# Kernel tuning notes

Hardware: AMD Instinct MI355X
Metric: run time of the kernel (lower is better)

The kernel has to match this reference:

```python
import jax, jax.numpy as jnp
import numpy as np

WH, WW = 8, 8          # window height/width
NUM_HEADS = 12


def _rel_tables():
    # continuous relative coords table, shape (1, 2*WH-1, 2*WW-1, 2)
    rh = np.arange(-(WH - 1), WH, dtype=np.float32)
    rw = np.arange(-(WW - 1), WW, dtype=np.float32)
    t = np.expand_dims(np.transpose(np.stack(np.meshgrid(rh, rw)), (1, 2, 0)), axis=0)
    t[:, :, :, 0] /= WH - 1
    t[:, :, :, 1] /= WW - 1
    t *= 8
    table = np.sign(t) * np.log2(np.abs(t) + 1.0) / np.log2(8)
    # relative position index, shape (WH*WW, WH*WW), values in [0, (2WH-1)*(2WW-1))
    ch = np.arange(WH)
    cw = np.arange(WW)
    x, y = np.meshgrid(ch, cw)
    coords = np.stack([y, x]).reshape(2, -1)
    rc = coords[:, :, None] - coords[:, None, :]
    rc = np.transpose(rc, (1, 2, 0))
    rc[:, :, 0] += WH - 1
    rc[:, :, 1] += WW - 1
    rc[:, :, 0] *= 2 * WW - 1
    idx = rc.sum(-1)
    return jnp.asarray(table, dtype=jnp.float32), jnp.asarray(idx, dtype=jnp.int32)


_REL_TABLE, _REL_IDX = _rel_tables()


def setup_inputs() -> dict:
    key = jax.random.key(0)
    ks = jax.random.split(key, 10)
    B_, N, C = 1152, 64, 384
    s = 1.0 / np.sqrt(C)
    return {
        "x": jax.random.normal(ks[0], (B_, N, C), jnp.float32),
        "mask": jnp.zeros((B_, N, N), jnp.float32),  # nW == B_ (B=1)
        "wq": jax.random.normal(ks[1], (C, C), jnp.float32) * s,
        "bq": jnp.zeros((C,), jnp.float32),
        "wk": jax.random.normal(ks[2], (C, C), jnp.float32) * s,
        "wv": jax.random.normal(ks[3], (C, C), jnp.float32) * s,
        "bv": jnp.zeros((C,), jnp.float32),
        "cpb_w1": jax.random.normal(ks[4], (2, 512), jnp.float32) * 0.5,
        "cpb_b1": jnp.zeros((512,), jnp.float32),
        "cpb_w2": jax.random.normal(ks[5], (512, NUM_HEADS), jnp.float32) * (1.0 / np.sqrt(512)),
        "cpb_b2": jnp.zeros((NUM_HEADS,), jnp.float32),
        "tau": jax.random.normal(ks[6], (1, NUM_HEADS, 1, 1), jnp.float32) * 0.02,
        "wproj": jax.random.normal(ks[7], (C, C), jnp.float32) * s,
        "bproj": jnp.zeros((C,), jnp.float32),
    }


def reference(x, mask, wq, bq, wk, wv, bv, cpb_w1, cpb_b1, cpb_w2, cpb_b2, tau, wproj, bproj):
    B_, N, C = x.shape
    H = NUM_HEADS
    Dh = C // H

    def heads(t):  # (B_, N, C) -> (B_, H, N, Dh)
        return jnp.transpose(t.reshape(B_, N, H, Dh), (0, 2, 1, 3))

    q = heads(x @ wq + bq)
    k = heads(x @ wk)
    v = heads(x @ wv + bv)

    # cosine attention: normalize by |q||k|, clamp denominator
    qn = jnp.linalg.norm(q, axis=-1)  # (B_, H, N)
    kn = jnp.linalg.norm(k, axis=-1)
    denom = jnp.maximum(qn[..., :, None] * kn[..., None, :], 1e-6)
    logit_scale = jnp.maximum(tau + jnp.log(10.0), 0.01)  # (1, H, 1, 1)
    attn = jnp.einsum('bhnd,bhmd->bhnm', q, k) / denom * logit_scale

    # continuous position bias via small MLP + gather by relative index
    tb = jax.nn.relu(_REL_TABLE @ cpb_w1 + cpb_b1) @ cpb_w2 + cpb_b2  # (1,15,15,H)
    tb = tb.reshape(-1, H)  # (225, H)
    bias = tb[_REL_IDX.reshape(-1)].reshape(N, N, H)
    bias = 16.0 * jax.nn.sigmoid(jnp.transpose(bias, (2, 0, 1)))  # (H, N, N)
    attn = attn + bias[None]

    nW = mask.shape[0]
    attn = (attn.reshape(B_ // nW, nW, H, N, N) + mask[None, :, None]).reshape(B_, H, N, N)
    attn = jax.nn.softmax(attn, axis=-1)

    out = jnp.transpose(jnp.einsum('bhnm,bhmd->bhnd', attn, v), (0, 2, 1, 3)).reshape(B_, N, C)
    return out @ wproj + bproj
```

## Files before the change

### kernel.cpp

```cpp
#include <hip/hip_runtime.h>
#include <math.h>

#define NB   1152
#define NTOK 64
#define NC   384
#define NH   12
#define NDH  32

typedef short short8 __attribute__((ext_vector_type(8)));
typedef float f32x4  __attribute__((ext_vector_type(4)));

__device__ __forceinline__ unsigned short f2bf(float f) {
    unsigned int u = __builtin_bit_cast(unsigned int, f);
    unsigned int r = u + 0x7fffu + ((u >> 16) & 1u);
    return (unsigned short)(r >> 16);
}
__device__ __forceinline__ unsigned int pack2(float lo, float hi) {
    return (unsigned int)f2bf(lo) | ((unsigned int)f2bf(hi) << 16);
}
__device__ __forceinline__ f32x4 mfma_bf16(short8 a, short8 b, f32x4 c) {
    return __builtin_amdgcn_mfma_f32_16x16x32_bf16(a, b, c, 0, 0, 0);
}

__device__ __forceinline__ short8 tile_afrag(const unsigned short* t, int row, int kq) {
    return *(const short8*)((const char*)t + row * 768 + ((kq ^ (row & 7)) << 4));
}

__device__ __forceinline__ short8 repack_frag(f32x4 a0, f32x4 a1, int Q, int t) {
    unsigned p00 = pack2(a0[0], a0[1]);
    unsigned p01 = pack2(a0[2], a0[3]);
    unsigned p10 = pack2(a1[0], a1[1]);
    unsigned p11 = pack2(a1[2], a1[3]);
    const int s0 = ((Q & 1) << 5) + t;
    const int s1 = s0 + 16;
    int u0a = __shfl((int)p00, s0, 64), u0b = __shfl((int)p10, s0, 64);
    int u1a = __shfl((int)p01, s0, 64), u1b = __shfl((int)p11, s0, 64);
    int u2a = __shfl((int)p00, s1, 64), u2b = __shfl((int)p10, s1, 64);
    int u3a = __shfl((int)p01, s1, 64), u3b = __shfl((int)p11, s1, 64);
    const bool hi = (Q & 2) != 0;
    uint4 u;
    u.x = (unsigned)(hi ? u0b : u0a);
    u.y = (unsigned)(hi ? u1b : u1a);
    u.z = (unsigned)(hi ? u2b : u2a);
    u.w = (unsigned)(hi ? u3b : u3a);
    return __builtin_bit_cast(short8, u);
}

__global__ __launch_bounds__(256) void prep_kernel(
    const float* __restrict__ wq, const float* __restrict__ wk,
    const float* __restrict__ wv, const float* __restrict__ wproj,
    unsigned int* __restrict__ wT, unsigned int* __restrict__ wprojT)
{
    const int o2 = blockIdx.x * 256 + threadIdx.x;
    if (o2 < 221184) {
        const int col = o2 / 192, k2 = o2 % 192, k = k2 * 2;
        const float* src = (col < 384) ? wq : ((col < 768) ? wk : wv);
        const int c = (col < 384) ? col : ((col < 768) ? col - 384 : col - 768);
        const float a = src[(size_t)k * NC + c];
        const float b = src[(size_t)(k + 1) * NC + c];
        wT[col * 192 + k2] = pack2(a, b);
    } else {
        const int o = o2 - 221184;
        const int col = o / 192, k2 = o % 192, k = k2 * 2;
        const float a = wproj[(size_t)k * NC + col];
        const float b = wproj[(size_t)(k + 1) * NC + col];
        wprojT[col * 192 + k2] = pack2(a, b);
    }
}

__global__ __launch_bounds__(64) void cpb_mlp_kernel(
    const float* __restrict__ w1, const float* __restrict__ b1,
    const float* __restrict__ w2, const float* __restrict__ b2,
    float* __restrict__ tbs)
{
    const int p = blockIdx.x;
    const int lane = threadIdx.x;
    const int ip = p / 15, jp = p % 15;
    float u0 = (float)(jp - 7) * (8.0f / 7.0f);
    float u1 = (float)(ip - 7) * (8.0f / 7.0f);
    float s0 = (u0 > 0.f) ? 1.f : ((u0 < 0.f) ? -1.f : 0.f);
    float s1 = (u1 > 0.f) ? 1.f : ((u1 < 0.f) ? -1.f : 0.f);
    float in0 = s0 * log2f(fabsf(u0) + 1.0f) * (1.0f / 3.0f);
    float in1 = s1 * log2f(fabsf(u1) + 1.0f) * (1.0f / 3.0f);

    float a[12];
    #pragma unroll
    for (int m = 0; m < 12; ++m) a[m] = 0.f;
    #pragma unroll
    for (int e = 0; e < 8; ++e) {
        const int j = lane * 8 + e;
        float hh = fmaxf(in0 * w1[j] + in1 * w1[512 + j] + b1[j], 0.0f);
        #pragma unroll
        for (int m = 0; m < 12; ++m) a[m] += hh * w2[j * 12 + m];
    }
    #pragma unroll
    for (int m = 0; m < 12; ++m) {
        #pragma unroll
        for (int off = 1; off < 64; off <<= 1) a[m] += __shfl_xor(a[m], off, 64);
    }
    if (lane < 12) tbs[p * 12 + lane] = a[lane] + b2[lane];
}

__global__ __launch_bounds__(1024) void bias_gather_kernel(
    const float* __restrict__ tbs, float* __restrict__ bias)
{
    const int i = blockIdx.x * 1024 + threadIdx.x;
    if (i >= NH * NTOK * NTOK) return;
    const int h = i >> 12, rem = i & 4095;
    const int ti = rem >> 6, tj = rem & 63;
    const int dr = (ti >> 3) - (tj >> 3);
    const int dc = (ti & 7) - (tj & 7);
    const int p = (dr + 7) * 15 + (dc + 7);
    bias[i] = 16.0f / (1.0f + __expf(-tbs[p * 12 + h]));
}

__global__ __launch_bounds__(256, 2) void attn_kernel(
    const float* __restrict__ x,    const float* __restrict__ mask,
    const float* __restrict__ bq,   const float* __restrict__ bv,
    const float* __restrict__ tau,  const unsigned short* __restrict__ wT,
    const float* __restrict__ bias, float* __restrict__ out)
{
    __shared__ unsigned short xs[64 * 384];
    __shared__ unsigned short vTs[4][32 * 72];
    __shared__ unsigned short Pss[4][16 * 72];

    const int tid = threadIdx.x;
    const int b   = blockIdx.x;
    const int w   = tid >> 6;
    const int lane = tid & 63;
    const int Q   = lane >> 4;
    const int t   = lane & 15;

    unsigned int* xsu = (unsigned int*)xs;

    float maskv[4][4];
    #pragma unroll
    for (int nt = 0; nt < 4; ++nt)
        #pragma unroll
        for (int r = 0; r < 4; ++r)
            maskv[nt][r] = mask[(size_t)b * 4096 + (Q * 4 + r) * 64 + nt * 16 + t];
    (void)maskv;

    {
        const int row = tid >> 2;
        const int q4  = tid & 3;
        const float* xr = &x[((size_t)b * NTOK + row) * NC + q4 * 96];
        #pragma unroll
        for (int e = 0; e < 24; ++e) {
            const float4 xv = *(const float4*)&xr[e * 4];
            const int p = q4 * 48 + e * 2;
            const int g = p >> 2;
            const int u = row * 192 + (((g ^ (row & 7)) << 2) | (p & 3));
            uint2 w2;
            w2.x = pack2(xv.x, xv.y);
            w2.y = pack2(xv.z, xv.w);
            *(uint2*)&xsu[u] = w2;
        }
    }
    __syncthreads();

    unsigned short* vT = vTs[w];
    unsigned short* Ps = Pss[w];

    for (int c = 0; c < 3; ++c) {
        const int h = w * 3 + c;

        f32x4 acckv[4][4];
        #pragma unroll
        for (int j = 0; j < 4; ++j)
            #pragma unroll
            for (int tt = 0; tt < 4; ++tt) acckv[j][tt] = (f32x4){0.f, 0.f, 0.f, 0.f};

        {
            const unsigned short* ap[4];
            #pragma unroll
            for (int j = 0; j < 4; ++j) {
                const int cbase = (1 + (j >> 1)) * 384 + h * 32 + (j & 1) * 16;
                ap[j] = wT + (size_t)(cbase + t) * NC + Q * 8;
            }
            for (int ks = 0; ks < 12; ++ks) {
                short8 bfr[4];
                #pragma unroll
                for (int tt = 0; tt < 4; ++tt)
                    bfr[tt] = tile_afrag(xs, tt * 16 + t, ks * 4 + Q);
                #pragma unroll
                for (int j = 0; j < 4; ++j) {
                    const short8 af = *(const short8*)&ap[j][ks * 32];
                    #pragma unroll
                    for (int tt = 0; tt < 4; ++tt)
                        acckv[j][tt] = mfma_bf16(af, bfr[tt], acckv[j][tt]);
                }
            }
        }

        #pragma unroll
        for (int a = 0; a < 2; ++a) {
            #pragma unroll
            for (int r = 0; r < 4; ++r) {
                const float bvv = bv[h * 32 + a * 16 + Q * 4 + r];
                #pragma unroll
                for (int tt = 0; tt < 4; ++tt)
                    vT[(a * 16 + Q * 4 + r) * 72 + tt * 16 + t]
                        = f2bf(acckv[2 + a][tt][r] + bvv);
            }
        }

        float kn[4];
        #pragma unroll
        for (int tt = 0; tt < 4; ++tt) {
            float sk = 0.f;
            #pragma unroll
            for (int a = 0; a < 2; ++a)
                #pragma unroll
                for (int r = 0; r < 4; ++r)
                    sk += acckv[a][tt][r] * acckv[a][tt][r];
            sk += __shfl_xor(sk, 16, 64);
            sk += __shfl_xor(sk, 32, 64);
            kn[tt] = sqrtf(sk);
        }

        short8 bk[4];
        #pragma unroll
        for (int nt = 0; nt < 4; ++nt)
            bk[nt] = repack_frag(acckv[0][nt], acckv[1][nt], Q, t);

        short8 vf[2][2];
        #pragma unroll
        for (int n = 0; n < 2; ++n)
            #pragma unroll
            for (int st = 0; st < 2; ++st)
                vf[n][st] = *(const short8*)&vT[(n * 16 + t) * 72 + st * 32 + Q * 8];

        f32x4 accq[2][4];
        #pragma unroll
        for (int a = 0; a < 2; ++a)
            #pragma unroll
            for (int tt = 0; tt < 4; ++tt) accq[a][tt] = (f32x4){0.f, 0.f, 0.f, 0.f};

        {
            const unsigned short* ap[2];
            #pragma unroll
            for (int a = 0; a < 2; ++a)
                ap[a] = wT + (size_t)(h * 32 + a * 16 + t) * NC + Q * 8;
            for (int ks = 0; ks < 12; ++ks) {
                short8 bfr[4];
                #pragma unroll
                for (int tt = 0; tt < 4; ++tt)
                    bfr[tt] = tile_afrag(xs, tt * 16 + t, ks * 4 + Q);
                #pragma unroll
                for (int a = 0; a < 2; ++a) {
                    const short8 af = *(const short8*)&ap[a][ks * 32];
                    #pragma unroll
                    for (int tt = 0; tt < 4; ++tt)
                        accq[a][tt] = mfma_bf16(af, bfr[tt], accq[a][tt]);
                }
            }
        }

        float qn[4];
        short8 aqf[4];
        #pragma unroll
        for (int a = 0; a < 2; ++a) {
            #pragma unroll
            for (int r = 0; r < 4; ++r) {
                const float bqv = bq[h * 32 + a * 16 + Q * 4 + r];
                #pragma unroll
                for (int tt = 0; tt < 4; ++tt) accq[a][tt][r] += bqv;
            }
        }
        #pragma unroll
        for (int tt = 0; tt < 4; ++tt) {
            float sq = 0.f;
            #pragma unroll
            for (int a = 0; a < 2; ++a)
                #pragma unroll
                for (int r = 0; r < 4; ++r)
                    sq += accq[a][tt][r] * accq[a][tt][r];
            sq += __shfl_xor(sq, 16, 64);
            sq += __shfl_xor(sq, 32, 64);
            qn[tt] = sqrtf(sq);
            aqf[tt] = repack_frag(accq[0][tt], accq[1][tt], Q, t);
        }

        const float ls = fmaxf(tau[h] + 2.302585093f, 0.01f);

        #pragma unroll
        for (int mt = 0; mt < 4; ++mt) {
            float bmv[4][4];
            #pragma unroll
            for (int nt = 0; nt < 4; ++nt)
                #pragma unroll
                for (int r = 0; r < 4; ++r) {
                    const int row = mt * 16 + Q * 4 + r;
                    const int col = nt * 16 + t;
                    bmv[nt][r] = bias[h * 4096 + row * 64 + col]
                               + mask[(size_t)b * 4096 + row * 64 + col];
                }

            float qr[4];
            #pragma unroll
            for (int r = 0; r < 4; ++r) qr[r] = __shfl(qn[mt], Q * 4 + r, 64);

            float svf[4][4];
            #pragma unroll
            for (int nt = 0; nt < 4; ++nt) {
                const f32x4 sv = mfma_bf16(aqf[mt], bk[nt], (f32x4){0.f, 0.f, 0.f, 0.f});
                #pragma unroll
                for (int r = 0; r < 4; ++r) {
                    const float den = fmaxf(qr[r] * kn[nt], 1e-6f);
                    svf[nt][r] = sv[r] / den * ls + bmv[nt][r];
                }
            }

            float mx[4], sm[4];
            #pragma unroll
            for (int r = 0; r < 4; ++r) {
                float m = fmaxf(fmaxf(svf[0][r], svf[1][r]), fmaxf(svf[2][r], svf[3][r]));
                #pragma unroll
                for (int off = 1; off < 16; off <<= 1) m = fmaxf(m, __shfl_xor(m, off, 64));
                mx[r] = m; sm[r] = 0.f;
            }
            #pragma unroll
            for (int nt = 0; nt < 4; ++nt)
                #pragma unroll
                for (int r = 0; r < 4; ++r) {
                    const float e = __expf(svf[nt][r] - mx[r]);
                    svf[nt][r] = e; sm[r] += e;
                }
            #pragma unroll
            for (int r = 0; r < 4; ++r) {
                #pragma unroll
                for (int off = 1; off < 16; off <<= 1) sm[r] += __shfl_xor(sm[r], off, 64);
            }

            #pragma unroll
            for (int nt = 0; nt < 4; ++nt)
                #pragma unroll
                for (int r = 0; r < 4; ++r)
                    Ps[(Q * 4 + r) * 72 + nt * 16 + t] = f2bf(svf[nt][r]);

            f32x4 oa[2];
            oa[0] = (f32x4){0.f, 0.f, 0.f, 0.f};
            oa[1] = (f32x4){0.f, 0.f, 0.f, 0.f};
            #pragma unroll
            for (int st = 0; st < 2; ++st) {
                const short8 apf = *(const short8*)&Ps[t * 72 + st * 32 + Q * 8];
                #pragma unroll
                for (int n = 0; n < 2; ++n)
                    oa[n] = mfma_bf16(apf, vf[n][st], oa[n]);
            }

            float rsi[4];
            #pragma unroll
            for (int r = 0; r < 4; ++r) rsi[r] = 1.0f / sm[r];
            #pragma unroll
            for (int n = 0; n < 2; ++n)
                #pragma unroll
                for (int r = 0; r < 4; ++r)
                    out[((size_t)b * NTOK + mt * 16 + Q * 4 + r) * NC + h * 32 + n * 16 + t]
                        = oa[n][r] * rsi[r];
        }
    }
}

__global__ __launch_bounds__(256) void proj_kernel(
    const unsigned short* __restrict__ wprojT, const float* __restrict__ bproj,
    float* __restrict__ out)
{
    __shared__ unsigned short as_[64 * 384];
    unsigned int* asu = (unsigned int*)as_;

    const int tid  = threadIdx.x;
    const size_t r0 = (size_t)blockIdx.x * 64;
    const int w    = tid >> 6;
    const int lane = tid & 63;
    const int quad = lane >> 4;
    const int lq   = lane & 15;

    {
        const int row = tid >> 2;
        const int q4  = tid & 3;
        const float* xr = &out[(r0 + row) * NC + q4 * 96];
        #pragma unroll
        for (int e = 0; e < 24; ++e) {
            const float4 xv = *(const float4*)&xr[e * 4];
            const int p = q4 * 48 + e * 2;
            const int g = p >> 2;
            const int u = row * 192 + (((g ^ (row & 7)) << 2) | (p & 3));
            uint2 w2;
            w2.x = pack2(xv.x, xv.y);
            w2.y = pack2(xv.z, xv.w);
            *(uint2*)&asu[u] = w2;
        }
    }
    __syncthreads();

    f32x4 acc[4][6];
    #pragma unroll
    for (int mt = 0; mt < 4; ++mt)
        #pragma unroll
        for (int n = 0; n < 6; ++n) acc[mt][n] = (f32x4){0.f, 0.f, 0.f, 0.f};

    const unsigned short* bp[6];
    #pragma unroll
    for (int n = 0; n < 6; ++n)
        bp[n] = wprojT + (size_t)(w * 96 + n * 16 + lq) * NC + quad * 8;

    for (int ksI = 0; ksI < 12; ++ksI) {
        short8 am[4];
        #pragma unroll
        for (int mt = 0; mt < 4; ++mt)
            am[mt] = tile_afrag(as_, mt * 16 + lq, ksI * 4 + quad);
        #pragma unroll
        for (int n = 0; n < 6; ++n) {
            const short8 bb = *(const short8*)&bp[n][ksI * 32];
            #pragma unroll
            for (int mt = 0; mt < 4; ++mt) acc[mt][n] = mfma_bf16(am[mt], bb, acc[mt][n]);
        }
    }

    float bpv[6];
    #pragma unroll
    for (int n = 0; n < 6; ++n) bpv[n] = bproj[w * 96 + n * 16 + lq];
    #pragma unroll
    for (int mt = 0; mt < 4; ++mt)
        #pragma unroll
        for (int n = 0; n < 6; ++n)
            #pragma unroll
            for (int r = 0; r < 4; ++r)
                out[(r0 + mt * 16 + quad * 4 + r) * NC + w * 96 + n * 16 + lq]
                    = acc[mt][n][r] + bpv[n];
}

extern "C" void kernel_launch(void* const* d_in, const int* in_sizes, int n_in,
                              void* d_out, int out_size, void* d_ws, size_t ws_size,
                              hipStream_t stream) {
    (void)in_sizes; (void)n_in; (void)out_size; (void)ws_size;
    const float* x     = (const float*)d_in[0];
    const float* mask  = (const float*)d_in[1];
    const float* wq    = (const float*)d_in[2];
    const float* bq    = (const float*)d_in[3];
    const float* wk    = (const float*)d_in[4];
    const float* wv    = (const float*)d_in[5];
    const float* bv    = (const float*)d_in[6];
    const float* w1    = (const float*)d_in[7];
    const float* b1    = (const float*)d_in[8];
    const float* w2    = (const float*)d_in[9];
    const float* b2    = (const float*)d_in[10];
    const float* tau   = (const float*)d_in[11];
    const float* wproj = (const float*)d_in[12];
    const float* bproj = (const float*)d_in[13];
    float* out = (float*)d_out;

    unsigned short* wT     = (unsigned short*)d_ws;
    unsigned short* wprojT = (unsigned short*)((char*)d_ws + 884736);
    float*          bias   = (float*)((char*)d_ws + 884736 + 294912);
    float*          tbs    = (float*)((char*)d_ws + 884736 + 294912 + 196608);

    prep_kernel<<<1152, 256, 0, stream>>>(wq, wk, wv, wproj,
                                          (unsigned int*)wT, (unsigned int*)wprojT);
    cpb_mlp_kernel<<<225, 64, 0, stream>>>(w1, b1, w2, b2, tbs);
    bias_gather_kernel<<<48, 1024, 0, stream>>>(tbs, bias);
    attn_kernel<<<NB, 256, 0, stream>>>(x, mask, bq, bv, tau, wT, bias, out);
    proj_kernel<<<NB, 256, 0, stream>>>(wprojT, bproj, out);
}
```

Measured before the change: 631.4 us.

## Compute attention in transposed MFMA layout to keep P and V in registers

The attention kernel now computes S^T, V^T and O^T by swapping MFMA operands. Each lane then owns a whole query row, so the softmax max and sum reductions shrink to two cross-lane shuffles, and P and V fragments are repacked in registers instead of going through per-wave LDS buffers. Bias and mask loads and output stores become float4-vectorised, and the occupancy hint rises from 2 to 3 blocks per CU. The trade-off is more repack work and register pressure, which could cause spills under the tighter launch bound.

Result: slower. 812.2 us (+28.6%).

```diff
diff --git a/kernel.cpp b/kernel.cpp
--- a/kernel.cpp
+++ b/kernel.cpp
@@ -114,32 +114,22 @@
     bias[i] = 16.0f / (1.0f + __expf(-tbs[p * 12 + h]));
 }
 
-__global__ __launch_bounds__(256, 2) void attn_kernel(
+__global__ __launch_bounds__(256, 3) void attn_kernel(
     const float* __restrict__ x,    const float* __restrict__ mask,
     const float* __restrict__ bq,   const float* __restrict__ bv,
     const float* __restrict__ tau,  const unsigned short* __restrict__ wT,
     const float* __restrict__ bias, float* __restrict__ out)
 {
     __shared__ unsigned short xs[64 * 384];
-    __shared__ unsigned short vTs[4][32 * 72];
-    __shared__ unsigned short Pss[4][16 * 72];
-
-    const int tid = threadIdx.x;
-    const int b   = blockIdx.x;
-    const int w   = tid >> 6;
+
+    const int tid  = threadIdx.x;
+    const int b    = blockIdx.x;
+    const int w    = tid >> 6;
     const int lane = tid & 63;
-    const int Q   = lane >> 4;
-    const int t   = lane & 15;
+    const int Q    = lane >> 4;
+    const int t    = lane & 15;
 
     unsigned int* xsu = (unsigned int*)xs;
-
-    float maskv[4][4];
-    #pragma unroll
-    for (int nt = 0; nt < 4; ++nt)
-        #pragma unroll
-        for (int r = 0; r < 4; ++r)
-            maskv[nt][r] = mask[(size_t)b * 4096 + (Q * 4 + r) * 64 + nt * 16 + t];
-    (void)maskv;
 
     {
         const int row = tid >> 2;
@@ -159,24 +149,22 @@
     }
     __syncthreads();
 
-    unsigned short* vT = vTs[w];
-    unsigned short* Ps = Pss[w];
-
     for (int c = 0; c < 3; ++c) {
         const int h = w * 3 + c;
 
-        f32x4 acckv[4][4];
+        f32x4 akv[4][4];
         #pragma unroll
         for (int j = 0; j < 4; ++j)
             #pragma unroll
-            for (int tt = 0; tt < 4; ++tt) acckv[j][tt] = (f32x4){0.f, 0.f, 0.f, 0.f};
+            for (int tt = 0; tt < 4; ++tt) akv[j][tt] = (f32x4){0.f, 0.f, 0.f, 0.f};
 
         {
-            const unsigned short* ap[4];
-            #pragma unroll
-            for (int j = 0; j < 4; ++j) {
-                const int cbase = (1 + (j >> 1)) * 384 + h * 32 + (j & 1) * 16;
-                ap[j] = wT + (size_t)(cbase + t) * NC + Q * 8;
+            const unsigned short* apk[2];
+            const unsigned short* apv[2];
+            #pragma unroll
+            for (int a = 0; a < 2; ++a) {
+                apk[a] = wT + (size_t)(384 + h * 32 + a * 16 + t) * NC + Q * 8;
+                apv[a] = wT + (size_t)(768 + h * 32 + a * 16 + t) * NC + Q * 8;
             }
             for (int ks = 0; ks < 12; ++ks) {
                 short8 bfr[4];
@@ -184,25 +172,29 @@
                 for (int tt = 0; tt < 4; ++tt)
                     bfr[tt] = tile_afrag(xs, tt * 16 + t, ks * 4 + Q);
                 #pragma unroll
-                for (int j = 0; j < 4; ++j) {
-                    const short8 af = *(const short8*)&ap[j][ks * 32];
+                for (int a = 0; a < 2; ++a) {
+                    const short8 afk = *(const short8*)&apk[a][ks * 32];
                     #pragma unroll
                     for (int tt = 0; tt < 4; ++tt)
-                        acckv[j][tt] = mfma_bf16(af, bfr[tt], acckv[j][tt]);
+                        akv[a][tt] = mfma_bf16(afk, bfr[tt], akv[a][tt]);
                 }
+                #pragma unroll
+                for (int a = 0; a < 2; ++a) {
+                    const short8 afv = *(const short8*)&apv[a][ks * 32];
+                    #pragma unroll
+                    for (int tt = 0; tt < 4; ++tt)
+                        akv[2 + a][tt] = mfma_bf16(bfr[tt], afv, akv[2 + a][tt]);
+                }
             }
         }
 
         #pragma unroll
         for (int a = 0; a < 2; ++a) {
-            #pragma unroll
-            for (int r = 0; r < 4; ++r) {
-                const float bvv = bv[h * 32 + a * 16 + Q * 4 + r];
-                #pragma unroll
-                for (int tt = 0; tt < 4; ++tt)
-                    vT[(a * 16 + Q * 4 + r) * 72 + tt * 16 + t]
-                        = f2bf(acckv[2 + a][tt][r] + bvv);
-            }
+            const float bvv = bv[h * 32 + a * 16 + t];
+            #pragma unroll
+            for (int tt = 0; tt < 4; ++tt)
+                #pragma unroll
+                for (int r = 0; r < 4; ++r) akv[2 + a][tt][r] += bvv;
         }
 
         float kn[4];
@@ -212,8 +204,7 @@
             #pragma unroll
             for (int a = 0; a < 2; ++a)
                 #pragma unroll
-                for (int r = 0; r < 4; ++r)
-                    sk += acckv[a][tt][r] * acckv[a][tt][r];
+                for (int r = 0; r < 4; ++r) sk += akv[a][tt][r] * akv[a][tt][r];
             sk += __shfl_xor(sk, 16, 64);
             sk += __shfl_xor(sk, 32, 64);
             kn[tt] = sqrtf(sk);
@@ -222,14 +213,20 @@
         short8 bk[4];
         #pragma unroll
         for (int nt = 0; nt < 4; ++nt)
-            bk[nt] = repack_frag(acckv[0][nt], acckv[1][nt], Q, t);
-
-        short8 vf[2][2];
+            bk[nt] = repack_frag(akv[0][nt], akv[1][nt], Q, t);
+        short8 vfrag[2][2];
         #pragma unroll
         for (int n = 0; n < 2; ++n)
             #pragma unroll
             for (int st = 0; st < 2; ++st)
-                vf[n][st] = *(const short8*)&vT[(n * 16 + t) * 72 + st * 32 + Q * 8];
+                vfrag[n][st] = repack_frag(akv[2 + n][2 * st], akv[2 + n][2 * st + 1], Q, t);
+
+        float knr[4][4];
+        #pragma unroll
+        for (int nt = 0; nt < 4; ++nt)
+            #pragma unroll
+            for (int r = 0; r < 4; ++r)
+                knr[nt][r] = __shfl(kn[nt], Q * 4 + r, 64);
 
         f32x4 accq[2][4];
         #pragma unroll
@@ -238,10 +235,10 @@
             for (int tt = 0; tt < 4; ++tt) accq[a][tt] = (f32x4){0.f, 0.f, 0.f, 0.f};
 
         {
-            const unsigned short* ap[2];
+            const unsigned short* apq[2];
             #pragma unroll
             for (int a = 0; a < 2; ++a)
-                ap[a] = wT + (size_t)(h * 32 + a * 16 + t) * NC + Q * 8;
+                apq[a] = wT + (size_t)(h * 32 + a * 16 + t) * NC + Q * 8;
             for (int ks = 0; ks < 12; ++ks) {
                 short8 bfr[4];
                 #pragma unroll
@@ -249,33 +246,31 @@
                     bfr[tt] = tile_afrag(xs, tt * 16 + t, ks * 4 + Q);
                 #pragma unroll
                 for (int a = 0; a < 2; ++a) {
-                    const short8 af = *(const short8*)&ap[a][ks * 32];
+                    const short8 afq = *(const short8*)&apq[a][ks * 32];
                     #pragma unroll
                     for (int tt = 0; tt < 4; ++tt)
-                        accq[a][tt] = mfma_bf16(af, bfr[tt], accq[a][tt]);
+                        accq[a][tt] = mfma_bf16(afq, bfr[tt], accq[a][tt]);
                 }
             }
         }
 
+        #pragma unroll
+        for (int a = 0; a < 2; ++a)
+            #pragma unroll
+            for (int r = 0; r < 4; ++r) {
+                const float bqv = bq[h * 32 + a * 16 + Q * 4 + r];
+                #pragma unroll
+                for (int tt = 0; tt < 4; ++tt) accq[a][tt][r] += bqv;
+            }
         float qn[4];
         short8 aqf[4];
         #pragma unroll
-        for (int a = 0; a < 2; ++a) {
-            #pragma unroll
-            for (int r = 0; r < 4; ++r) {
-                const float bqv = bq[h * 32 + a * 16 + Q * 4 + r];
-                #pragma unroll
-                for (int tt = 0; tt < 4; ++tt) accq[a][tt][r] += bqv;
-            }
-        }
-        #pragma unroll
         for (int tt = 0; tt < 4; ++tt) {
             float sq = 0.f;
             #pragma unroll
             for (int a = 0; a < 2; ++a)
                 #pragma unroll
-                for (int r = 0; r < 4; ++r)
-                    sq += accq[a][tt][r] * accq[a][tt][r];
+                for (int r = 0; r < 4; ++r) sq += accq[a][tt][r] * accq[a][tt][r];
             sq += __shfl_xor(sq, 16, 64);
             sq += __shfl_xor(sq, 32, 64);
             qn[tt] = sqrtf(sq);
@@ -286,79 +281,67 @@
 
         #pragma unroll
         for (int mt = 0; mt < 4; ++mt) {
-            float bmv[4][4];
+            const float* bro = &bias[h * 4096 + (mt * 16 + t) * 64];
+            const float* mro = &mask[(size_t)b * 4096 + (mt * 16 + t) * 64];
+            f32x4 bm[4];
             #pragma unroll
             for (int nt = 0; nt < 4; ++nt)
+                bm[nt] = *(const f32x4*)&bro[nt * 16 + Q * 4]
+                       + *(const f32x4*)&mro[nt * 16 + Q * 4];
+
+            f32x4 sT[4];
+            #pragma unroll
+            for (int nt = 0; nt < 4; ++nt)
+                sT[nt] = mfma_bf16(bk[nt], aqf[mt], (f32x4){0.f, 0.f, 0.f, 0.f});
+            #pragma unroll
+            for (int nt = 0; nt < 4; ++nt)
                 #pragma unroll
                 for (int r = 0; r < 4; ++r) {
-                    const int row = mt * 16 + Q * 4 + r;
-                    const int col = nt * 16 + t;
-                    bmv[nt][r] = bias[h * 4096 + row * 64 + col]
-                               + mask[(size_t)b * 4096 + row * 64 + col];
+                    const float den = fmaxf(qn[mt] * knr[nt][r], 1e-6f);
+                    sT[nt][r] = sT[nt][r] / den * ls + bm[nt][r];
                 }
 
-            float qr[4];
-            #pragma unroll
-            for (int r = 0; r < 4; ++r) qr[r] = __shfl(qn[mt], Q * 4 + r, 64);
-
-            float svf[4][4];
+            float mnt[4];
+            #pragma unroll
+            for (int nt = 0; nt < 4; ++nt)
+                mnt[nt] = fmaxf(fmaxf(sT[nt][0], sT[nt][1]), fmaxf(sT[nt][2], sT[nt][3]));
+            float mx = fmaxf(fmaxf(mnt[0], mnt[1]), fmaxf(mnt[2], mnt[3]));
+            mx = fmaxf(mx, __shfl_xor(mx, 16, 64));
+            mx = fmaxf(mx, __shfl_xor(mx, 32, 64));
+
+            float snt[4];
             #pragma unroll
             for (int nt = 0; nt < 4; ++nt) {
-                const f32x4 sv = mfma_bf16(aqf[mt], bk[nt], (f32x4){0.f, 0.f, 0.f, 0.f});
-                #pragma unroll
-                for (int r = 0; r < 4; ++r) {
-                    const float den = fmaxf(qr[r] * kn[nt], 1e-6f);
-                    svf[nt][r] = sv[r] / den * ls + bmv[nt][r];
-                }
-            }
-
-            float mx[4], sm[4];
-            #pragma unroll
-            for (int r = 0; r < 4; ++r) {
-                float m = fmaxf(fmaxf(svf[0][r], svf[1][r]), fmaxf(svf[2][r], svf[3][r]));
-                #pragma unroll
-                for (int off = 1; off < 16; off <<= 1) m = fmaxf(m, __shfl_xor(m, off, 64));
-                mx[r] = m; sm[r] = 0.f;
-            }
-            #pragma unroll
-            for (int nt = 0; nt < 4; ++nt)
-                #pragma unroll
-                for (int r = 0; r < 4; ++r) {
-                    const float e = __expf(svf[nt][r] - mx[r]);
-                    svf[nt][r] = e; sm[r] += e;
-                }
-            #pragma unroll
-            for (int r = 0; r < 4; ++r) {
-                #pragma unroll
-                for (int off = 1; off < 16; off <<= 1) sm[r] += __shfl_xor(sm[r], off, 64);
-            }
-
-            #pragma unroll
-            for (int nt = 0; nt < 4; ++nt)
-                #pragma unroll
-                for (int r = 0; r < 4; ++r)
-                    Ps[(Q * 4 + r) * 72 + nt * 16 + t] = f2bf(svf[nt][r]);
+                #pragma unroll
+                for (int r = 0; r < 4; ++r) sT[nt][r] = __expf(sT[nt][r] - mx);
+                snt[nt] = (sT[nt][0] + sT[nt][1]) + (sT[nt][2] + sT[nt][3]);
+            }
+            float sm = (snt[0] + snt[1]) + (snt[2] + snt[3]);
+            sm += __shfl_xor(sm, 16, 64);
+            sm += __shfl_xor(sm, 32, 64);
+
+            const short8 pf0 = repack_frag(sT[0], sT[1], Q, t);
+            const short8 pf1 = repack_frag(sT[2], sT[3], Q, t);
 
             f32x4 oa[2];
             oa[0] = (f32x4){0.f, 0.f, 0.f, 0.f};
             oa[1] = (f32x4){0.f, 0.f, 0.f, 0.f};
             #pragma unroll
-            for (int st = 0; st < 2; ++st) {
-                const short8 apf = *(const short8*)&Ps[t * 72 + st * 32 + Q * 8];
-                #pragma unroll
-                for (int n = 0; n < 2; ++n)
-                    oa[n] = mfma_bf16(apf, vf[n][st], oa[n]);
-            }
-
-            float rsi[4];
-            #pragma unroll
-            for (int r = 0; r < 4; ++r) rsi[r] = 1.0f / sm[r];
-            #pragma unroll
-            for (int n = 0; n < 2; ++n)
-                #pragma unroll
-                for (int r = 0; r < 4; ++r)
-                    out[((size_t)b * NTOK + mt * 16 + Q * 4 + r) * NC + h * 32 + n * 16 + t]
-                        = oa[n][r] * rsi[r];
+            for (int n = 0; n < 2; ++n) {
+                oa[n] = mfma_bf16(vfrag[n][0], pf0, oa[n]);
+                oa[n] = mfma_bf16(vfrag[n][1], pf1, oa[n]);
+            }
+
+            const float rsi = 1.0f / sm;
+            #pragma unroll
+            for (int n = 0; n < 2; ++n) {
+                float4 o4;
+                o4.x = oa[n][0] * rsi;
+                o4.y = oa[n][1] * rsi;
+                o4.z = oa[n][2] * rsi;
+                o4.w = oa[n][3] * rsi;
+                *(float4*)&out[((size_t)b * NTOK + mt * 16 + t) * NC + h * 32 + n * 16 + Q * 4] = o4;
+            }
         }
     }
 }
```
